# Kernel tuning notes

Hardware: AMD Instinct MI355X
Metric: run time of the kernel (lower is better)

## Reference

```python
import jax, jax.numpy as jnp
import numpy as np

DIM, E, K, H = 1024, 8, 2, 4096

def setup_inputs() -> dict:
    key = jax.random.key(0)
    ks = jax.random.split(key, 5)
    s_in = 1.0 / np.sqrt(DIM)
    s_h = 1.0 / np.sqrt(H)
    return {
        "x": jax.random.normal(ks[0], (4, 2048, DIM), dtype=jnp.float32),
        "Wr": jax.random.normal(ks[1], (DIM, E), dtype=jnp.float32) * s_in,
        "W1": jax.random.normal(ks[2], (E, DIM, H), dtype=jnp.float32) * s_in,
        "b1": jnp.zeros((E, H), dtype=jnp.float32),
        "W2": jax.random.normal(ks[3], (E, H, DIM), dtype=jnp.float32) * s_h,
        "b2": jnp.zeros((E, DIM), dtype=jnp.float32),
    }

def reference(x, Wr, W1, b1, W2, b2):
    batch, seq, dim = x.shape
    x_flat = x.reshape(-1, dim)                      # [T, D]
    logits = x_flat @ Wr                             # [T, E]
    w, ind = jax.lax.top_k(logits, K)                # [T, K]
    w = jax.nn.softmax(w, axis=-1)
    # combine[t, e] = sum_i w[t, i] * (ind[t, i] == e)
    combine = jnp.einsum('tke,tk->te', jax.nn.one_hot(ind, E, dtype=x.dtype), w)  # [T, E]

    def body(acc, params):
        W1e, b1e, W2e, b2e, ce = params
        h = jax.nn.gelu(x_flat @ W1e + b1e, approximate=False)  # exact GELU (torch nn.GELU default)
        y = h @ W2e + b2e                                        # [T, D]
        return acc + ce[:, None] * y, None

    out0 = jnp.zeros_like(x_flat)
    out, _ = jax.lax.scan(body, out0, (W1, b1, W2, b2, combine.T))
    return out.reshape(batch, seq, dim)
```

## Files before the change

### kernel.cpp

```cpp
#include <hip/hip_runtime.h>
#include <hip/hip_bf16.h>

#define TDIM 1024
#define NEXP 8
#define NHID 4096

typedef __hip_bfloat16 bf16;
typedef __attribute__((ext_vector_type(8))) short bf16x8;
typedef __attribute__((ext_vector_type(4))) float f32x4;

__device__ __forceinline__ void gload_lds16(void* lds, const void* g) {
  __builtin_amdgcn_global_load_lds(
      (const __attribute__((address_space(1))) unsigned int*)g,
      (__attribute__((address_space(3))) unsigned int*)lds, 16, 0, 0);
}

__device__ __forceinline__ unsigned short f2bf_bits(float f) {
  __hip_bfloat16 b = __float2bfloat16(f);
  unsigned short u;
  __builtin_memcpy(&u, &b, 2);
  return u;
}

__global__ void cvt_x_kernel(const float* __restrict__ x, bf16* __restrict__ xb, int n4) {
  int i = blockIdx.x * blockDim.x + threadIdx.x;
  if (i >= n4) return;
  float4 v = reinterpret_cast<const float4*>(x)[i];
  ushort4 o;
  o.x = f2bf_bits(v.x);
  o.y = f2bf_bits(v.y);
  o.z = f2bf_bits(v.z);
  o.w = f2bf_bits(v.w);
  reinterpret_cast<ushort4*>(xb)[i] = o;
}

__global__ void transpose_cvt_kernel(const float* __restrict__ in, bf16* __restrict__ out,
                                     int R, int C) {
  __shared__ float tile[32][33];
  const size_t eoff = (size_t)blockIdx.z * R * C;
  const float* src = in + eoff;
  bf16* dst = out + eoff;
  int c0 = blockIdx.x * 32, r0 = blockIdx.y * 32;
  int tx = threadIdx.x, ty = threadIdx.y;
#pragma unroll
  for (int i = 0; i < 32; i += 8)
    tile[ty + i][tx] = src[(size_t)(r0 + ty + i) * C + (c0 + tx)];
  __syncthreads();
#pragma unroll
  for (int i = 0; i < 32; i += 8)
    dst[(size_t)(c0 + ty + i) * R + (r0 + tx)] = __float2bfloat16(tile[tx][ty + i]);
}

__global__ void router_kernel(const float* __restrict__ x, const float* __restrict__ Wr,
                              int* __restrict__ idx, float* __restrict__ wtok,
                              int* __restrict__ cnt, int T) {
  int wave = (blockIdx.x * blockDim.x + threadIdx.x) >> 6;
  int lane = threadIdx.x & 63;
  if (wave >= T) return;
  const float* xr = x + (size_t)wave * TDIM;
  float acc[NEXP];
#pragma unroll
  for (int e = 0; e < NEXP; ++e) acc[e] = 0.f;
#pragma unroll
  for (int i = 0; i < TDIM / 64; ++i) {
    float xv = xr[lane + i * 64];
    const float* wr = Wr + (size_t)(lane + i * 64) * NEXP;
#pragma unroll
    for (int e = 0; e < NEXP; ++e) acc[e] += xv * wr[e];
  }
#pragma unroll
  for (int e = 0; e < NEXP; ++e) {
    float v = acc[e];
#pragma unroll
    for (int s = 32; s; s >>= 1) v += __shfl_xor(v, s);
    acc[e] = v;
  }
  if (lane == 0) {
    int e0 = 0;
    float l0 = acc[0];
    for (int e = 1; e < NEXP; ++e)
      if (acc[e] > l0) { l0 = acc[e]; e0 = e; }
    int e1 = -1;
    float l1 = -INFINITY;
    for (int e = 0; e < NEXP; ++e)
      if (e != e0 && acc[e] > l1) { l1 = acc[e]; e1 = e; }
    float z = __expf(l1 - l0);
    float w0 = 1.f / (1.f + z);
    float w1 = z / (1.f + z);
    idx[wave * 2] = e0;
    idx[wave * 2 + 1] = e1;
    wtok[wave * 2] = w0;
    wtok[wave * 2 + 1] = w1;
    atomicAdd(&cnt[e0], 1);
    atomicAdd(&cnt[e1], 1);
  }
}

__global__ void scan_kernel(const int* __restrict__ cnt, int* __restrict__ offs) {
  if (threadIdx.x == 0 && blockIdx.x == 0) {
    int s = 0;
    for (int e = 0; e < NEXP; ++e) { offs[e] = s; s += cnt[e]; }
  }
}

__global__ void build_perm_kernel(const int* __restrict__ idx, const float* __restrict__ wtok,
                                  const int* __restrict__ offs, int* __restrict__ fill,
                                  int* __restrict__ perm, float* __restrict__ wgrp, int T) {
  int t = blockIdx.x * blockDim.x + threadIdx.x;
  if (t >= T) return;
#pragma unroll
  for (int k = 0; k < 2; ++k) {
    int e = idx[t * 2 + k];
    int p = offs[e] + atomicAdd(&fill[e], 1);
    perm[p] = t;
    wgrp[p] = wtok[t * 2 + k];
  }
}

template <int KD, int ND, bool GATHER, bool SCATTER>
__global__ __launch_bounds__(256) void moe_gemm(
    const bf16* __restrict__ A, const bf16* __restrict__ BT, const float* __restrict__ bias,
    const int* __restrict__ perm, const float* __restrict__ wgrp, const int* __restrict__ cnt,
    const int* __restrict__ offs, bf16* __restrict__ Hout, float* __restrict__ Out) {
  __shared__ short sA[128 * 32];
  __shared__ short sB[128 * 32];
  const int e = blockIdx.z;
  const int ce = cnt[e];
  const int m0 = blockIdx.y * 128;
  if (m0 >= ce) return;
  const int base = offs[e];
  const int n0 = blockIdx.x * 128;
  const int tid = threadIdx.x;
  const int wid = tid >> 6;
  const int lane = tid & 63;

  const int srow = tid >> 2;
  const int sch = (tid & 3) * 8;
  const bf16 *aP0, *aP1;
  {
    int g0 = m0 + srow;
    if (g0 > ce - 1) g0 = ce - 1;
    int g1 = m0 + 64 + srow;
    if (g1 > ce - 1) g1 = ce - 1;
    if (GATHER) {
      aP0 = A + (size_t)perm[base + g0] * KD + sch;
      aP1 = A + (size_t)perm[base + g1] * KD + sch;
    } else {
      aP0 = A + (size_t)(base + g0) * KD + sch;
      aP1 = A + (size_t)(base + g1) * KD + sch;
    }
  }
  const bf16* bP0 = BT + ((size_t)e * ND + n0 + srow) * KD + sch;
  const bf16* bP1 = bP0 + (size_t)64 * KD;

  char* sAw = (char*)sA + wid * 1024;
  char* sBw = (char*)sB + wid * 1024;

  const int wm = wid >> 1, wn = wid & 1;
  const int lcol = lane & 15;
  const int lkg = (lane >> 4) * 8;
  const short* paBase = sA + (size_t)(wm * 64 + lcol) * 32 + lkg;
  const short* pbBase = sB + (size_t)(wn * 64 + lcol) * 32 + lkg;

  f32x4 acc[4][4];
#pragma unroll
  for (int m = 0; m < 4; ++m)
#pragma unroll
    for (int n = 0; n < 4; ++n) acc[m][n] = (f32x4){0.f, 0.f, 0.f, 0.f};

  for (int k0 = 0; k0 < KD; k0 += 32) {
    gload_lds16(sAw, aP0 + k0);
    gload_lds16(sAw + 4096, aP1 + k0);
    gload_lds16(sBw, bP0 + k0);
    gload_lds16(sBw + 4096, bP1 + k0);
    __syncthreads();
    bf16x8 af[4], bfr[4];
#pragma unroll
    for (int m = 0; m < 4; ++m) af[m] = *(const bf16x8*)(paBase + m * 16 * 32);
#pragma unroll
    for (int n = 0; n < 4; ++n) bfr[n] = *(const bf16x8*)(pbBase + n * 16 * 32);
#pragma unroll
    for (int m = 0; m < 4; ++m)
#pragma unroll
      for (int n = 0; n < 4; ++n)
        acc[m][n] = __builtin_amdgcn_mfma_f32_16x16x32_bf16(af[m], bfr[n], acc[m][n], 0, 0, 0);
    __syncthreads();
  }

  const int lr4 = (lane >> 4) * 4;
  if (SCATTER) {
#pragma unroll
    for (int m = 0; m < 4; ++m)
#pragma unroll
      for (int r = 0; r < 4; ++r) {
        int grow = m0 + wm * 64 + m * 16 + lr4 + r;
        if (grow < ce) {
          int tok = perm[base + grow];
          float wv = wgrp[base + grow];
          float* orow = Out + (size_t)tok * ND;
#pragma unroll
          for (int n = 0; n < 4; ++n) {
            int col = n0 + wn * 64 + n * 16 + lcol;
            float v = acc[m][n][r] + bias[e * ND + col];
            atomicAdd(orow + col, wv * v);
          }
        }
      }
  } else {
#pragma unroll
    for (int m = 0; m < 4; ++m)
#pragma unroll
      for (int r = 0; r < 4; ++r) {
        int grow = m0 + wm * 64 + m * 16 + lr4 + r;
        if (grow < ce) {
          bf16* hrow = Hout + (size_t)(base + grow) * ND;
#pragma unroll
          for (int n = 0; n < 4; ++n) {
            int col = n0 + wn * 64 + n * 16 + lcol;
            float v = acc[m][n][r] + bias[e * ND + col];
            float g = 0.5f * v * (1.0f + erff(v * 0.70710678118654752f));
            hrow[col] = __float2bfloat16(g);
          }
        }
      }
  }
}

extern "C" void kernel_launch(void* const* d_in, const int* in_sizes, int n_in, void* d_out,
                              int out_size, void* d_ws, size_t ws_size, hipStream_t stream) {
  const float* x = (const float*)d_in[0];
  const float* Wr = (const float*)d_in[1];
  const float* W1 = (const float*)d_in[2];
  const float* b1 = (const float*)d_in[3];
  const float* W2 = (const float*)d_in[4];
  const float* b2 = (const float*)d_in[5];
  float* out = (float*)d_out;
  const int T = in_sizes[0] / TDIM;

  size_t off = 0;
  auto alloc = [&](size_t bytes) {
    void* q = (char*)d_ws + off;
    off += (bytes + 255) & ~(size_t)255;
    return q;
  };
  bf16* xb = (bf16*)alloc((size_t)T * TDIM * 2);
  bf16* W1T = (bf16*)alloc((size_t)NEXP * TDIM * NHID * 2);
  bf16* W2T = (bf16*)alloc((size_t)NEXP * TDIM * NHID * 2);
  bf16* h = (bf16*)alloc((size_t)2 * T * NHID * 2);
  int* idx = (int*)alloc((size_t)T * 2 * 4);
  float* wtok = (float*)alloc((size_t)T * 2 * 4);
  int* perm = (int*)alloc((size_t)T * 2 * 4);
  float* wgrp = (float*)alloc((size_t)T * 2 * 4);
  int* cnt = (int*)alloc(256);
  int* fill = cnt + 8;
  int* offs = cnt + 16;

  hipMemsetAsync(d_out, 0, (size_t)out_size * 4, stream);
  hipMemsetAsync(cnt, 0, 64, stream);

  cvt_x_kernel<<<(T * TDIM / 4 + 255) / 256, 256, 0, stream>>>(x, xb, T * TDIM / 4);
  transpose_cvt_kernel<<<dim3(NHID / 32, TDIM / 32, NEXP), dim3(32, 8), 0, stream>>>(W1, W1T, TDIM,
                                                                                     NHID);
  transpose_cvt_kernel<<<dim3(TDIM / 32, NHID / 32, NEXP), dim3(32, 8), 0, stream>>>(W2, W2T, NHID,
                                                                                     TDIM);
  router_kernel<<<T / 4, 256, 0, stream>>>(x, Wr, idx, wtok, cnt, T);
  scan_kernel<<<1, 64, 0, stream>>>(cnt, offs);
  build_perm_kernel<<<(T + 255) / 256, 256, 0, stream>>>(idx, wtok, offs, fill, perm, wgrp, T);

  moe_gemm<TDIM, NHID, true, false>
      <<<dim3(NHID / 128, (T + 127) / 128, NEXP), 256, 0, stream>>>(xb, W1T, b1, perm, wgrp, cnt,
                                                                    offs, h, nullptr);
  moe_gemm<NHID, TDIM, false, true>
      <<<dim3(TDIM / 128, (T + 127) / 128, NEXP), 256, 0, stream>>>(h, W2T, b2, perm, wgrp, cnt,
                                                                    offs, nullptr, out);
}
```

Measured before the change: 943.0 us.

## Use 256x256 double-buffered MoE GEMM tiles and replace atomic scatter with combine pass

The expert GEMM tile grows from 128x128 to 256x256 with 512 threads, a K-step of 64 and double-buffered LDS loads, so the next tile's global-to-LDS copy overlaps the MFMAs. A 1D grid is remapped across experts, and the W2 GEMM now writes bf16 per-slot rows into the reused W1T buffer instead of issuing fp32 atomicAdds into the output. A new combine kernel does the weighted two-expert sum per token, which also removes the output memset. The weight transpose kernel gets 64x64 tiles with vectorised loads and stores, and the router uses float4 loads. Rounding the second GEMM's output to bf16 before combining costs some precision, and the larger tiles use about 128KB of LDS per block, which lowers occupancy and wastes work on partially filled expert tiles.

Result: slower. 1.084 ms (+14.9%).

```diff
diff --git a/kernel.cpp b/kernel.cpp
--- a/kernel.cpp
+++ b/kernel.cpp
@@ -7,6 +7,7 @@
 
 typedef __hip_bfloat16 bf16;
 typedef __attribute__((ext_vector_type(8))) short bf16x8;
+typedef __attribute__((ext_vector_type(8))) unsigned short u16x8;
 typedef __attribute__((ext_vector_type(4))) float f32x4;
 
 __device__ __forceinline__ void gload_lds16(void* lds, const void* g) {
@@ -20,6 +21,12 @@
   unsigned short u;
   __builtin_memcpy(&u, &b, 2);
   return u;
+}
+
+__device__ __forceinline__ float bf2f(unsigned short u) {
+  union { unsigned int i; float f; } c;
+  c.i = ((unsigned int)u) << 16;
+  return c.f;
 }
 
 __global__ void cvt_x_kernel(const float* __restrict__ x, bf16* __restrict__ xb, int n4) {
@@ -34,21 +41,34 @@
   reinterpret_cast<ushort4*>(xb)[i] = o;
 }
 
-__global__ void transpose_cvt_kernel(const float* __restrict__ in, bf16* __restrict__ out,
-                                     int R, int C) {
-  __shared__ float tile[32][33];
+__global__ __launch_bounds__(256) void transpose_cvt_kernel(const float* __restrict__ in,
+                                                            bf16* __restrict__ out, int R, int C) {
+  __shared__ float tile[64][65];
   const size_t eoff = (size_t)blockIdx.z * R * C;
   const float* src = in + eoff;
   bf16* dst = out + eoff;
-  int c0 = blockIdx.x * 32, r0 = blockIdx.y * 32;
-  int tx = threadIdx.x, ty = threadIdx.y;
-#pragma unroll
-  for (int i = 0; i < 32; i += 8)
-    tile[ty + i][tx] = src[(size_t)(r0 + ty + i) * C + (c0 + tx)];
+  const int c0 = blockIdx.x * 64, r0 = blockIdx.y * 64;
+  const int tid = threadIdx.x;
+#pragma unroll
+  for (int i = 0; i < 4; ++i) {
+    int s = tid + i * 256;
+    int r = s >> 4, cg = (s & 15) * 4;
+    float4 v = *reinterpret_cast<const float4*>(src + (size_t)(r0 + r) * C + c0 + cg);
+    tile[r][cg] = v.x;
+    tile[r][cg + 1] = v.y;
+    tile[r][cg + 2] = v.z;
+    tile[r][cg + 3] = v.w;
+  }
   __syncthreads();
 #pragma unroll
-  for (int i = 0; i < 32; i += 8)
-    dst[(size_t)(c0 + ty + i) * R + (r0 + tx)] = __float2bfloat16(tile[tx][ty + i]);
+  for (int i = 0; i < 2; ++i) {
+    int s = tid + i * 256;
+    int c = s >> 3, rg = (s & 7) * 8;
+    u16x8 o;
+#pragma unroll
+    for (int j = 0; j < 8; ++j) o[j] = f2bf_bits(tile[rg + j][c]);
+    *reinterpret_cast<u16x8*>(dst + (size_t)(c0 + c) * R + r0 + rg) = o;
+  }
 }
 
 __global__ void router_kernel(const float* __restrict__ x, const float* __restrict__ Wr,
@@ -57,16 +77,29 @@
   int wave = (blockIdx.x * blockDim.x + threadIdx.x) >> 6;
   int lane = threadIdx.x & 63;
   if (wave >= T) return;
-  const float* xr = x + (size_t)wave * TDIM;
+  const float4* xr4 = reinterpret_cast<const float4*>(x + (size_t)wave * TDIM);
+  const float4* wr4 = reinterpret_cast<const float4*>(Wr);
   float acc[NEXP];
 #pragma unroll
   for (int e = 0; e < NEXP; ++e) acc[e] = 0.f;
 #pragma unroll
-  for (int i = 0; i < TDIM / 64; ++i) {
-    float xv = xr[lane + i * 64];
-    const float* wr = Wr + (size_t)(lane + i * 64) * NEXP;
-#pragma unroll
-    for (int e = 0; e < NEXP; ++e) acc[e] += xv * wr[e];
+  for (int i = 0; i < TDIM / 256; ++i) {
+    float4 xv = xr4[lane + i * 64];
+    int row = (lane + i * 64) * 4;
+#pragma unroll
+    for (int j = 0; j < 4; ++j) {
+      float xs = (&xv.x)[j];
+      float4 wa = wr4[(row + j) * 2];
+      float4 wb = wr4[(row + j) * 2 + 1];
+      acc[0] += xs * wa.x;
+      acc[1] += xs * wa.y;
+      acc[2] += xs * wa.z;
+      acc[3] += xs * wa.w;
+      acc[4] += xs * wb.x;
+      acc[5] += xs * wb.y;
+      acc[6] += xs * wb.z;
+      acc[7] += xs * wb.w;
+    }
   }
 #pragma unroll
   for (int e = 0; e < NEXP; ++e) {
@@ -103,9 +136,9 @@
   }
 }
 
-__global__ void build_perm_kernel(const int* __restrict__ idx, const float* __restrict__ wtok,
-                                  const int* __restrict__ offs, int* __restrict__ fill,
-                                  int* __restrict__ perm, float* __restrict__ wgrp, int T) {
+__global__ void build_perm_kernel(const int* __restrict__ idx, const int* __restrict__ offs,
+                                  int* __restrict__ fill, int* __restrict__ perm,
+                                  int* __restrict__ islot, int T) {
   int t = blockIdx.x * blockDim.x + threadIdx.x;
   if (t >= T) return;
 #pragma unroll
@@ -113,117 +146,134 @@
     int e = idx[t * 2 + k];
     int p = offs[e] + atomicAdd(&fill[e], 1);
     perm[p] = t;
-    wgrp[p] = wtok[t * 2 + k];
-  }
-}
-
-template <int KD, int ND, bool GATHER, bool SCATTER>
-__global__ __launch_bounds__(256) void moe_gemm(
+    islot[t * 2 + k] = p;
+  }
+}
+
+template <int KD, int ND, bool GATHER, bool GELU>
+__global__ __launch_bounds__(512, 2) void moe_gemm(
     const bf16* __restrict__ A, const bf16* __restrict__ BT, const float* __restrict__ bias,
-    const int* __restrict__ perm, const float* __restrict__ wgrp, const int* __restrict__ cnt,
-    const int* __restrict__ offs, bf16* __restrict__ Hout, float* __restrict__ Out) {
-  __shared__ short sA[128 * 32];
-  __shared__ short sB[128 * 32];
-  const int e = blockIdx.z;
+    const int* __restrict__ perm, const int* __restrict__ cnt, const int* __restrict__ offs,
+    bf16* __restrict__ Dst, int nm, int nn) {
+  __shared__ short sA[2][256 * 64];
+  __shared__ short sB[2][256 * 64];
+
+  const int nwg = NEXP * nm * nn;
+  const int bid = blockIdx.x;
+  const int wg = (bid & 7) * (nwg >> 3) + (bid >> 3);
+  const int e = wg / (nm * nn);
+  const int rem = wg % (nm * nn);
+  const int mb = rem / nn, nb = rem % nn;
+
   const int ce = cnt[e];
-  const int m0 = blockIdx.y * 128;
+  const int m0 = mb * 256;
   if (m0 >= ce) return;
   const int base = offs[e];
-  const int n0 = blockIdx.x * 128;
+  const int n0 = nb * 256;
   const int tid = threadIdx.x;
+  const int lane = tid & 63;
   const int wid = tid >> 6;
-  const int lane = tid & 63;
-
-  const int srow = tid >> 2;
-  const int sch = (tid & 3) * 8;
-  const bf16 *aP0, *aP1;
-  {
-    int g0 = m0 + srow;
-    if (g0 > ce - 1) g0 = ce - 1;
-    int g1 = m0 + 64 + srow;
-    if (g1 > ce - 1) g1 = ce - 1;
-    if (GATHER) {
-      aP0 = A + (size_t)perm[base + g0] * KD + sch;
-      aP1 = A + (size_t)perm[base + g1] * KD + sch;
-    } else {
-      aP0 = A + (size_t)(base + g0) * KD + sch;
-      aP1 = A + (size_t)(base + g1) * KD + sch;
-    }
-  }
-  const bf16* bP0 = BT + ((size_t)e * ND + n0 + srow) * KD + sch;
-  const bf16* bP1 = bP0 + (size_t)64 * KD;
-
-  char* sAw = (char*)sA + wid * 1024;
-  char* sBw = (char*)sB + wid * 1024;
-
-  const int wm = wid >> 1, wn = wid & 1;
+  const int wm = wid >> 2, wn = wid & 3;
+
+  const int trow = tid >> 3;
+  const int tk = (tid & 7) * 8;
+  const bf16* aSrc[4];
+  const bf16* bSrc[4];
+#pragma unroll
+  for (int i = 0; i < 4; ++i) {
+    int g = m0 + trow + i * 64;
+    if (g > ce - 1) g = ce - 1;
+    size_t arow = GATHER ? (size_t)perm[base + g] : (size_t)(base + g);
+    aSrc[i] = A + arow * KD + tk;
+    bSrc[i] = BT + ((size_t)e * ND + n0 + trow + i * 64) * KD + tk;
+  }
+
+  f32x4 acc[8][4];
+#pragma unroll
+  for (int m = 0; m < 8; ++m)
+#pragma unroll
+    for (int n = 0; n < 4; ++n) acc[m][n] = (f32x4){0.f, 0.f, 0.f, 0.f};
+
   const int lcol = lane & 15;
   const int lkg = (lane >> 4) * 8;
-  const short* paBase = sA + (size_t)(wm * 64 + lcol) * 32 + lkg;
-  const short* pbBase = sB + (size_t)(wn * 64 + lcol) * 32 + lkg;
-
-  f32x4 acc[4][4];
-#pragma unroll
-  for (int m = 0; m < 4; ++m)
-#pragma unroll
-    for (int n = 0; n < 4; ++n) acc[m][n] = (f32x4){0.f, 0.f, 0.f, 0.f};
-
-  for (int k0 = 0; k0 < KD; k0 += 32) {
-    gload_lds16(sAw, aP0 + k0);
-    gload_lds16(sAw + 4096, aP1 + k0);
-    gload_lds16(sBw, bP0 + k0);
-    gload_lds16(sBw + 4096, bP1 + k0);
+
+#pragma unroll
+  for (int i = 0; i < 4; ++i) {
+    gload_lds16((char*)sA[0] + tid * 16 + i * 8192, aSrc[i]);
+    gload_lds16((char*)sB[0] + tid * 16 + i * 8192, bSrc[i]);
+  }
+  __syncthreads();
+
+  const int NT = KD / 64;
+  for (int kt = 0; kt < NT; ++kt) {
+    const int cur = kt & 1;
+    if (kt + 1 < NT) {
+      const int k0 = (kt + 1) * 64;
+#pragma unroll
+      for (int i = 0; i < 4; ++i) {
+        gload_lds16((char*)sA[cur ^ 1] + tid * 16 + i * 8192, aSrc[i] + k0);
+        gload_lds16((char*)sB[cur ^ 1] + tid * 16 + i * 8192, bSrc[i] + k0);
+      }
+    }
+    const short* sAb = sA[cur];
+    const short* sBb = sB[cur];
+    bf16x8 bfr[8];
+#pragma unroll
+    for (int n = 0; n < 4; ++n)
+#pragma unroll
+      for (int kk = 0; kk < 2; ++kk)
+        bfr[n * 2 + kk] =
+            *(const bf16x8*)(sBb + ((wn * 64 + n * 16 + lcol) * 64 + kk * 32 + lkg));
+#pragma unroll
+    for (int m = 0; m < 8; ++m) {
+      const short* ap = sAb + ((wm * 128 + m * 16 + lcol) * 64 + lkg);
+      bf16x8 a0 = *(const bf16x8*)(ap);
+      bf16x8 a1 = *(const bf16x8*)(ap + 32);
+#pragma unroll
+      for (int n = 0; n < 4; ++n) {
+        acc[m][n] = __builtin_amdgcn_mfma_f32_16x16x32_bf16(a0, bfr[n * 2], acc[m][n], 0, 0, 0);
+        acc[m][n] = __builtin_amdgcn_mfma_f32_16x16x32_bf16(a1, bfr[n * 2 + 1], acc[m][n], 0, 0, 0);
+      }
+    }
     __syncthreads();
-    bf16x8 af[4], bfr[4];
-#pragma unroll
-    for (int m = 0; m < 4; ++m) af[m] = *(const bf16x8*)(paBase + m * 16 * 32);
-#pragma unroll
-    for (int n = 0; n < 4; ++n) bfr[n] = *(const bf16x8*)(pbBase + n * 16 * 32);
-#pragma unroll
-    for (int m = 0; m < 4; ++m)
-#pragma unroll
-      for (int n = 0; n < 4; ++n)
-        acc[m][n] = __builtin_amdgcn_mfma_f32_16x16x32_bf16(af[m], bfr[n], acc[m][n], 0, 0, 0);
-    __syncthreads();
-  }
-
+  }
+
+  float bv[4];
+#pragma unroll
+  for (int n = 0; n < 4; ++n) bv[n] = bias[e * ND + n0 + wn * 64 + n * 16 + lcol];
   const int lr4 = (lane >> 4) * 4;
-  if (SCATTER) {
-#pragma unroll
-    for (int m = 0; m < 4; ++m)
-#pragma unroll
-      for (int r = 0; r < 4; ++r) {
-        int grow = m0 + wm * 64 + m * 16 + lr4 + r;
-        if (grow < ce) {
-          int tok = perm[base + grow];
-          float wv = wgrp[base + grow];
-          float* orow = Out + (size_t)tok * ND;
-#pragma unroll
-          for (int n = 0; n < 4; ++n) {
-            int col = n0 + wn * 64 + n * 16 + lcol;
-            float v = acc[m][n][r] + bias[e * ND + col];
-            atomicAdd(orow + col, wv * v);
-          }
+#pragma unroll
+  for (int m = 0; m < 8; ++m)
+#pragma unroll
+    for (int r = 0; r < 4; ++r) {
+      int grow = m0 + wm * 128 + m * 16 + lr4 + r;
+      if (grow < ce) {
+        bf16* drow = Dst + (size_t)(base + grow) * ND;
+#pragma unroll
+        for (int n = 0; n < 4; ++n) {
+          int col = n0 + wn * 64 + n * 16 + lcol;
+          float v = acc[m][n][r] + bv[n];
+          if (GELU) v = 0.5f * v * (1.0f + erff(v * 0.70710678118654752f));
+          drow[col] = __float2bfloat16(v);
         }
       }
-  } else {
-#pragma unroll
-    for (int m = 0; m < 4; ++m)
-#pragma unroll
-      for (int r = 0; r < 4; ++r) {
-        int grow = m0 + wm * 64 + m * 16 + lr4 + r;
-        if (grow < ce) {
-          bf16* hrow = Hout + (size_t)(base + grow) * ND;
-#pragma unroll
-          for (int n = 0; n < 4; ++n) {
-            int col = n0 + wn * 64 + n * 16 + lcol;
-            float v = acc[m][n][r] + bias[e * ND + col];
-            float g = 0.5f * v * (1.0f + erff(v * 0.70710678118654752f));
-            hrow[col] = __float2bfloat16(g);
-          }
-        }
-      }
-  }
+    }
+}
+
+__global__ void combine_kernel(const bf16* __restrict__ y, const int* __restrict__ islot,
+                               const float* __restrict__ wtok, float* __restrict__ out) {
+  const int t = blockIdx.x;
+  const int d = threadIdx.x * 4;
+  const int s0 = islot[t * 2], s1 = islot[t * 2 + 1];
+  const float w0 = wtok[t * 2], w1 = wtok[t * 2 + 1];
+  ushort4 ya = *reinterpret_cast<const ushort4*>(y + (size_t)s0 * TDIM + d);
+  ushort4 yb = *reinterpret_cast<const ushort4*>(y + (size_t)s1 * TDIM + d);
+  float4 o;
+  o.x = w0 * bf2f(ya.x) + w1 * bf2f(yb.x);
+  o.y = w0 * bf2f(ya.y) + w1 * bf2f(yb.y);
+  o.z = w0 * bf2f(ya.z) + w1 * bf2f(yb.z);
+  o.w = w0 * bf2f(ya.w) + w1 * bf2f(yb.w);
+  *reinterpret_cast<float4*>(out + (size_t)t * TDIM + d) = o;
 }
 
 extern "C" void kernel_launch(void* const* d_in, const int* in_sizes, int n_in, void* d_out,
@@ -250,27 +300,25 @@
   int* idx = (int*)alloc((size_t)T * 2 * 4);
   float* wtok = (float*)alloc((size_t)T * 2 * 4);
   int* perm = (int*)alloc((size_t)T * 2 * 4);
-  float* wgrp = (float*)alloc((size_t)T * 2 * 4);
+  int* islot = (int*)alloc((size_t)T * 2 * 4);
   int* cnt = (int*)alloc(256);
   int* fill = cnt + 8;
   int* offs = cnt + 16;
-
-  hipMemsetAsync(d_out, 0, (size_t)out_size * 4, stream);
+  bf16* y = W1T;
+
   hipMemsetAsync(cnt, 0, 64, stream);
 
   cvt_x_kernel<<<(T * TDIM / 4 + 255) / 256, 256, 0, stream>>>(x, xb, T * TDIM / 4);
-  transpose_cvt_kernel<<<dim3(NHID / 32, TDIM / 32, NEXP), dim3(32, 8), 0, stream>>>(W1, W1T, TDIM,
-                                                                                     NHID);
-  transpose_cvt_kernel<<<dim3(TDIM / 32, NHID / 32, NEXP), dim3(32, 8), 0, stream>>>(W2, W2T, NHID,
-                                                                                     TDIM);
+  transpose_cvt_kernel<<<dim3(NHID / 64, TDIM / 64, NEXP), 256, 0, stream>>>(W1, W1T, TDIM, NHID);
+  transpose_cvt_kernel<<<dim3(TDIM / 64, NHID / 64, NEXP), 256, 0, stream>>>(W2, W2T, NHID, TDIM);
   router_kernel<<<T / 4, 256, 0, stream>>>(x, Wr, idx, wtok, cnt, T);
   scan_kernel<<<1, 64, 0, stream>>>(cnt, offs);
-  build_perm_kernel<<<(T + 255) / 256, 256, 0, stream>>>(idx, wtok, offs, fill, perm, wgrp, T);
-
-  moe_gemm<TDIM, NHID, true, false>
-      <<<dim3(NHID / 128, (T + 127) / 128, NEXP), 256, 0, stream>>>(xb, W1T, b1, perm, wgrp, cnt,
-                                                                    offs, h, nullptr);
-  moe_gemm<NHID, TDIM, false, true>
-      <<<dim3(TDIM / 128, (T + 127) / 128, NEXP), 256, 0, stream>>>(h, W2T, b2, perm, wgrp, cnt,
-                                                                    offs, nullptr, out);
-}
+  build_perm_kernel<<<(T + 255) / 256, 256, 0, stream>>>(idx, offs, fill, perm, islot, T);
+
+  moe_gemm<TDIM, NHID, true, true><<<NEXP * 32 * 16, 512, 0, stream>>>(
+      xb, W1T, b1, perm, cnt, offs, h, 32, 16);
+  moe_gemm<NHID, TDIM, false, false><<<NEXP * 32 * 4, 512, 0, stream>>>(
+      h, W2T, b2, perm, cnt, offs, y, 32, 4);
+
+  combine_kernel<<<T, 256, 0, stream>>>(y, islot, wtok, out);
+}
```
